# Optimization experiments

Hardware: AMD Instinct MI355X
Metric: run time of the kernel (lower is better)

Reference implementation:

```python
import jax, jax.numpy as jnp
import numpy as np

N = 4096
IN_C = 256
F = 256          # num_filter
C = 40           # label_dim
KP1 = 3          # K+1 Chebyshev orders (K=2 hardcoded in forward)
E = 131072
TWO_PI = 2.0 * np.pi


def build_Lc(edges, q, edge_weight, n):
    """Conjugate of the normalized magnetic Laplacian (max_eigen=2 => L = -A_n * exp(i*Theta)).
    We return conj(L) because the original code swaps L.real/L.imag when feeding `process`,
    which is algebraically O_i = i * conj(T_i(L))."""
    row, col = edges[0], edges[1]
    A = jnp.zeros((n, n), jnp.float32).at[row, col].add(edge_weight)  # duplicates sum, as in coo_matrix
    A_sym = 0.5 * (A + A.T)
    d = A_sym.sum(axis=0)
    d = jnp.where(d == 0, 1.0, d)
    dinv = d ** -0.5
    A_n = dinv[:, None] * A_sym * dinv[None, :]
    Theta = TWO_PI * q * (A - A.T)
    # conj(L) = -A_n * exp(-i*Theta)
    return (-A_n).astype(jnp.complex64) * jnp.exp(-1j * Theta.astype(jnp.complex64))


def cheb_layer(Lc, Xr, Xi, W, b):
    """One ChebConv_Qin_Direct layer. Output = sum_i (i * T_i(conj(L)) @ Xc) @ W_i + bias,
    which reproduces the real/imag-swapped `process` of the original module."""
    Xc = (Xr + 1j * Xi).astype(jnp.complex64)      # [N, d]
    Z0 = Xc
    Z1 = Lc @ Xc                                   # sparse-equivalent spmm, dense here
    Z2 = 2.0 * (Lc @ Z1) - Z0                      # Chebyshev recursion T2 = 2 L T1 - T0
    Yc = 1j * (Z0 @ W[0].astype(jnp.complex64)
               + Z1 @ W[1].astype(jnp.complex64)
               + Z2 @ W[2].astype(jnp.complex64))  # [N, out]
    return Yc.real + b, Yc.imag + b


def setup_inputs() -> dict:
    key = jax.random.key(0)
    k = jax.random.split(key, 8)
    stdv1 = 1.0 / np.sqrt(F)
    return {
        "real": jax.random.normal(k[0], (N, IN_C), jnp.float32),
        "imag": jax.random.normal(k[1], (N, IN_C), jnp.float32),
        "edges": jax.random.randint(k[2], (2, E), 0, N),
        "q": jnp.float32(0.25),
        "edge_weight": jax.random.uniform(k[3], (E,), jnp.float32),
        "W1": jax.random.uniform(k[4], (KP1, IN_C, F), jnp.float32, -stdv1, stdv1),
        "b1": jnp.zeros((1, F), jnp.float32),
        "W2": jax.random.uniform(k[5], (KP1, F, F), jnp.float32, -stdv1, stdv1),
        "b2": jnp.zeros((1, F), jnp.float32),
        "Wc": jax.random.normal(k[6], (C, 2 * F), jnp.float32) * (1.0 / np.sqrt(2 * F)),
        "bc": jnp.zeros((C,), jnp.float32),
    }


def reference(real, imag, edges, q, edge_weight, W1, b1, W2, b2, Wc, bc):
    n = real.shape[0]
    Lc = build_Lc(edges, q, edge_weight, n)        # same L is rebuilt each layer in the original
    r, i = cheb_layer(Lc, real, imag, W1, b1)
    r, i = cheb_layer(Lc, r, i, W2, b2)            # activation=False, dropout=False
    x = jnp.concatenate([r, i], axis=-1)           # [N, 2F]
    logits = x @ Wc.T + bc                         # Conv1d(kernel_size=1) == linear
    return jax.nn.log_softmax(logits, axis=-1)     # [N, C]
```

## Files before the change

kernel.cpp:

```cpp
#include <hip/hip_runtime.h>
#include <cmath>

#define N_NODES 4096
#define FDIM    256
#define CDIM    40
#define NEDGE   131072
#define CAP     256
#define HBITS   19
#define HSIZE   (1 << HBITS)
#define TWO_PI_F 6.28318530717958647692f

typedef __bf16 bf16;
typedef __bf16 bf16x2 __attribute__((ext_vector_type(2)));
typedef __bf16 bf16x4 __attribute__((ext_vector_type(4)));
typedef __bf16 bf16x8 __attribute__((ext_vector_type(8)));
typedef _Float16 f16;
typedef _Float16 f16x2 __attribute__((ext_vector_type(2)));
typedef float  f32x4  __attribute__((ext_vector_type(4)));
typedef unsigned char u8;

static constexpr size_t NF = (size_t)N_NODES * FDIM;

struct __align__(16) Entry { unsigned ab, ba; int col, pad; };

__device__ __forceinline__ unsigned pack_h2(float a, float b) {
    f16x2 h; h[0] = (f16)a; h[1] = (f16)b;
    return __builtin_bit_cast(unsigned, h);
}
__device__ __forceinline__ f16x2 bch2(unsigned u) {
    return __builtin_bit_cast(f16x2, u);
}

__device__ __forceinline__ unsigned f32_to_e5m2(float v) {
    unsigned short h = __builtin_bit_cast(unsigned short, (f16)v);
    return ((unsigned)h + 0x7Fu + (((unsigned)h >> 8) & 1u)) >> 8 & 0xFFu;
}

__device__ __forceinline__ f16x2 e5m2_pair_lo(unsigned u) {
    return bch2(__builtin_amdgcn_perm(u, 0u, 0x05000400u));
}
__device__ __forceinline__ f16x2 e5m2_pair_hi(unsigned u) {
    return bch2(__builtin_amdgcn_perm(u, 0u, 0x07000600u));
}

__device__ __forceinline__ float fdot2(f16x2 a, f16x2 b, float c) {
#if __has_builtin(__builtin_amdgcn_fdot2)
    return __builtin_amdgcn_fdot2(a, b, c, false);
#else
    asm("v_dot2_f32_f16 %0, %1, %2, %0" : "+v"(c) : "v"(a), "v"(b));
    return c;
#endif
}

__device__ __forceinline__ void gld_lds16(const bf16* g, bf16* s) {
    __builtin_amdgcn_global_load_lds(
        (const __attribute__((address_space(1))) void*)g,
        (__attribute__((address_space(3))) void*)s,
        16, 0, 0);
}

__device__ __forceinline__ unsigned cell_hash(unsigned cell) {
    return (cell * 2654435761u) >> (32 - HBITS);
}

__global__ void hash_insert(const int* __restrict__ edges,
                            const float* __restrict__ ew,
                            int* __restrict__ hkey, float* __restrict__ hval,
                            float* __restrict__ rowsum, float* __restrict__ colsum) {
    int e = blockIdx.x * blockDim.x + threadIdx.x;
    if (e >= NEDGE) return;
    int r = edges[e], c = edges[NEDGE + e];
    float wv = ew[e];
    atomicAdd(rowsum + r, wv);
    atomicAdd(colsum + c, wv);
    unsigned cell = (unsigned)r * N_NODES + c;
    unsigned h = cell_hash(cell);
    for (;;) {
        int old = atomicCAS(hkey + h, 0, (int)(cell + 1));
        if (old == 0 || old == (int)(cell + 1)) { atomicAdd(hval + h, wv); break; }
        h = (h + 1) & (HSIZE - 1);
    }
}

__global__ __launch_bounds__(256) void hash_to_ell(
    const int* __restrict__ hkey, const float* __restrict__ hval,
    const float* __restrict__ rowsum, const float* __restrict__ colsum,
    const float* __restrict__ qptr,
    int* __restrict__ cnt, Entry* __restrict__ ent) {
    int h = blockIdx.x * 256 + threadIdx.x;
    int k = hkey[h];
    if (k == 0) return;
    unsigned cell = (unsigned)(k - 1);
    int i = cell >> 12, j = cell & 4095;
    float a = hval[h];
    float b = 0.f;
    bool mirror = false;
    if (i == j) { b = a; mirror = true; }
    else {
        unsigned mcell = (unsigned)j * N_NODES + i;
        unsigned hh = cell_hash(mcell);
        for (;;) {
            int kk = hkey[hh];
            if (kk == (int)(mcell + 1)) { b = hval[hh]; mirror = true; break; }
            if (kk == 0) break;
            hh = (hh + 1) & (HSIZE - 1);
        }
    }
    float di = 0.5f * (rowsum[i] + colsum[i]); if (di == 0.f) di = 1.f;
    float dj = 0.5f * (rowsum[j] + colsum[j]); if (dj == 0.f) dj = 1.f;
    float an = 0.5f * (a + b) / sqrtf(di * dj);
    float s, c;
    sincosf(TWO_PI_F * qptr[0] * (a - b), &s, &c);
    float lr = -an * c;
    float li = an * s;
    int pos = atomicAdd(cnt + i, 1);
    if (pos < CAP) {
        Entry en; en.ab = pack_h2(lr, -li); en.ba = pack_h2(li, lr);
        en.col = j; en.pad = 0;
        ent[(size_t)i * CAP + pos] = en;
    }
    if (!mirror) {
        int pos2 = atomicAdd(cnt + j, 1);
        if (pos2 < CAP) {
            Entry en; en.ab = pack_h2(lr, li); en.ba = pack_h2(-li, lr);
            en.col = i; en.pad = 0;
            ent[(size_t)j * CAP + pos2] = en;
        }
    }
}

#define NWT (256 * 768)
#define CAST_W_BLOCKS ((2 * NWT + 48 * 512) / 256)
__global__ __launch_bounds__(256) void cast_all(
    const float* __restrict__ Xr, const float* __restrict__ Xi,
    const float* __restrict__ W1, const float* __restrict__ W2,
    const float* __restrict__ Wc,
    bf16* __restrict__ Xr16, bf16* __restrict__ Xi16, u8* __restrict__ XC8,
    bf16* __restrict__ W1t, bf16* __restrict__ W2t, bf16* __restrict__ Wcb) {
    int bid = blockIdx.x;
    if (bid < (int)(NF / 256)) {
        int idx = bid * 256 + threadIdx.x;
        float vr = Xr[idx], vi = Xi[idx];
        Xr16[idx] = (bf16)vr; Xi16[idx] = (bf16)vi;
        unsigned pr = f32_to_e5m2(vr), pi = f32_to_e5m2(vi);
        ((unsigned short*)XC8)[idx] = (unsigned short)(pr | (pi << 8));
    } else {
        int idx = (bid - (int)(NF / 256)) * 256 + threadIdx.x;
        if (idx < 2 * NWT) {
            const float* W = (idx < NWT) ? W1 : W2;
            bf16* Wt = (idx < NWT) ? W1t : W2t;
            int id = (idx < NWT) ? idx : idx - NWT;
            int nout = id / 768, kk = id - nout * 768;
            int o = kk >> 8, k = kk & 255;
            Wt[id] = (bf16)W[((size_t)o * 256 + k) * 256 + nout];
        } else {
            int id = idx - 2 * NWT;
            int row = id >> 9, k = id & 511;
            Wcb[id] = (row < CDIM) ? (bf16)Wc[row * 512 + k] : (bf16)0.f;
        }
    }
}

__global__ __launch_bounds__(256) void spmm_k(
    const int* __restrict__ cnt, const Entry* __restrict__ ent,
    const u8* __restrict__ XC8,
    const bf16* __restrict__ C0r, const bf16* __restrict__ C0i,
    float alpha, float beta,
    bf16* __restrict__ Zr, bf16* __restrict__ Zi, u8* __restrict__ ZC8)
{
    __shared__ f32x4 redR[3][64];
    __shared__ f32x4 redI[3][64];

    const int wave = threadIdx.x >> 6, lane = threadIdx.x & 63;
    const int row = blockIdx.x;
    int n1 = cnt[row]; if (n1 > CAP) n1 = CAP;
    const Entry* erow = ent + (size_t)row * CAP;

    float ar[4] = {}, ai[4] = {};
    int e = wave;
    for (; e + 12 < n1; e += 16) {
        Entry e0 = erow[e];
        Entry e1 = erow[e + 4];
        Entry e2 = erow[e + 8];
        Entry e3 = erow[e + 12];
        uint2 x0 = *(const uint2*)&XC8[(size_t)(e0.col & 4095) * 512 + lane * 8];
        uint2 x1 = *(const uint2*)&XC8[(size_t)(e1.col & 4095) * 512 + lane * 8];
        uint2 x2 = *(const uint2*)&XC8[(size_t)(e2.col & 4095) * 512 + lane * 8];
        uint2 x3 = *(const uint2*)&XC8[(size_t)(e3.col & 4095) * 512 + lane * 8];
        {
            f16x2 ab = bch2(e0.ab), ba = bch2(e0.ba);
            f16x2 c0 = e5m2_pair_lo(x0.x), c1 = e5m2_pair_hi(x0.x);
            f16x2 c2 = e5m2_pair_lo(x0.y), c3 = e5m2_pair_hi(x0.y);
            ar[0] = fdot2(ab, c0, ar[0]); ai[0] = fdot2(ba, c0, ai[0]);
            ar[1] = fdot2(ab, c1, ar[1]); ai[1] = fdot2(ba, c1, ai[1]);
            ar[2] = fdot2(ab, c2, ar[2]); ai[2] = fdot2(ba, c2, ai[2]);
            ar[3] = fdot2(ab, c3, ar[3]); ai[3] = fdot2(ba, c3, ai[3]);
        }
        {
            f16x2 ab = bch2(e1.ab), ba = bch2(e1.ba);
            f16x2 c0 = e5m2_pair_lo(x1.x), c1 = e5m2_pair_hi(x1.x);
            f16x2 c2 = e5m2_pair_lo(x1.y), c3 = e5m2_pair_hi(x1.y);
            ar[0] = fdot2(ab, c0, ar[0]); ai[0] = fdot2(ba, c0, ai[0]);
            ar[1] = fdot2(ab, c1, ar[1]); ai[1] = fdot2(ba, c1, ai[1]);
            ar[2] = fdot2(ab, c2, ar[2]); ai[2] = fdot2(ba, c2, ai[2]);
            ar[3] = fdot2(ab, c3, ar[3]); ai[3] = fdot2(ba, c3, ai[3]);
        }
        {
            f16x2 ab = bch2(e2.ab), ba = bch2(e2.ba);
            f16x2 c0 = e5m2_pair_lo(x2.x), c1 = e5m2_pair_hi(x2.x);
            f16x2 c2 = e5m2_pair_lo(x2.y), c3 = e5m2_pair_hi(x2.y);
            ar[0] = fdot2(ab, c0, ar[0]); ai[0] = fdot2(ba, c0, ai[0]);
            ar[1] = fdot2(ab, c1, ar[1]); ai[1] = fdot2(ba, c1, ai[1]);
            ar[2] = fdot2(ab, c2, ar[2]); ai[2] = fdot2(ba, c2, ai[2]);
            ar[3] = fdot2(ab, c3, ar[3]); ai[3] = fdot2(ba, c3, ai[3]);
        }
        {
            f16x2 ab = bch2(e3.ab), ba = bch2(e3.ba);
            f16x2 c0 = e5m2_pair_lo(x3.x), c1 = e5m2_pair_hi(x3.x);
            f16x2 c2 = e5m2_pair_lo(x3.y), c3 = e5m2_pair_hi(x3.y);
            ar[0] = fdot2(ab, c0, ar[0]); ai[0] = fdot2(ba, c0, ai[0]);
            ar[1] = fdot2(ab, c1, ar[1]); ai[1] = fdot2(ba, c1, ai[1]);
            ar[2] = fdot2(ab, c2, ar[2]); ai[2] = fdot2(ba, c2, ai[2]);
            ar[3] = fdot2(ab, c3, ar[3]); ai[3] = fdot2(ba, c3, ai[3]);
        }
    }
    for (; e < n1; e += 4) {
        Entry e0 = erow[e];
        uint2 x0 = *(const uint2*)&XC8[(size_t)(e0.col & 4095) * 512 + lane * 8];
        f16x2 ab = bch2(e0.ab), ba = bch2(e0.ba);
        f16x2 c0 = e5m2_pair_lo(x0.x), c1 = e5m2_pair_hi(x0.x);
        f16x2 c2 = e5m2_pair_lo(x0.y), c3 = e5m2_pair_hi(x0.y);
        ar[0] = fdot2(ab, c0, ar[0]); ai[0] = fdot2(ba, c0, ai[0]);
        ar[1] = fdot2(ab, c1, ar[1]); ai[1] = fdot2(ba, c1, ai[1]);
        ar[2] = fdot2(ab, c2, ar[2]); ai[2] = fdot2(ba, c2, ai[2]);
        ar[3] = fdot2(ab, c3, ar[3]); ai[3] = fdot2(ba, c3, ai[3]);
    }

    if (wave != 0) {
        f32x4 r, i;
        #pragma unroll
        for (int c = 0; c < 4; ++c) { r[c] = ar[c]; i[c] = ai[c]; }
        redR[wave - 1][lane] = r;
        redI[wave - 1][lane] = i;
    }
    __syncthreads();
    if (wave != 0) return;

    #pragma unroll
    for (int w = 0; w < 3; ++w) {
        f32x4 r = redR[w][lane], i = redI[w][lane];
        #pragma unroll
        for (int c = 0; c < 4; ++c) { ar[c] += r[c]; ai[c] += i[c]; }
    }

    size_t pbase = (size_t)row * FDIM + lane * 4;
    float vr[4], vi[4];
    if (beta != 0.f) {
        bf16x4 cr = *(const bf16x4*)&C0r[pbase];
        bf16x4 ci = *(const bf16x4*)&C0i[pbase];
        #pragma unroll
        for (int c = 0; c < 4; ++c) {
            vr[c] = alpha * ar[c] + beta * (float)cr[c];
            vi[c] = alpha * ai[c] + beta * (float)ci[c];
        }
    } else {
        #pragma unroll
        for (int c = 0; c < 4; ++c) { vr[c] = alpha * ar[c]; vi[c] = alpha * ai[c]; }
    }
    bf16x4 pr, pi;
    #pragma unroll
    for (int c = 0; c < 4; ++c) { pr[c] = (bf16)vr[c]; pi[c] = (bf16)vi[c]; }
    *(bf16x4*)&Zr[pbase] = pr;
    *(bf16x4*)&Zi[pbase] = pi;
    if (ZC8) {
        uint2 o;
        o.x = f32_to_e5m2(vr[0]) | (f32_to_e5m2(vi[0]) << 8) |
              (f32_to_e5m2(vr[1]) << 16) | (f32_to_e5m2(vi[1]) << 24);
        o.y = f32_to_e5m2(vr[2]) | (f32_to_e5m2(vi[2]) << 8) |
              (f32_to_e5m2(vr[3]) << 16) | (f32_to_e5m2(vi[3]) << 24);
        *(uint2*)&ZC8[(size_t)row * 512 + lane * 8] = o;
    }
}

__global__ __launch_bounds__(256) void wapply_mfma(
    const bf16* __restrict__ Z0r, const bf16* __restrict__ Z0i,
    const bf16* __restrict__ Z1r, const bf16* __restrict__ Z1i,
    const bf16* __restrict__ Z2r, const bf16* __restrict__ Z2i,
    const bf16* __restrict__ Wt,
    const float* __restrict__ bias,
    bf16* __restrict__ O16r_r, bf16* __restrict__ O16r_i,
    u8* __restrict__ OC8)
{
    __shared__ __align__(16) bf16 sZr[32 * 32];
    __shared__ __align__(16) bf16 sZi[32 * 32];
    __shared__ __align__(16) bf16 sW [64 * 32];

    const int tid  = threadIdx.x;
    const int wave = tid >> 6;
    const int lane = tid & 63;
    const int rowBase = blockIdx.y * 32;
    const int colBase = blockIdx.x * 64;

    const int srow = lane >> 2;
    const int skc  = (lane & 3) * 8;

    f32x4 accSr[2] = {}, accSi[2] = {};
    const int fr = lane & 15;
    const int fk = (lane >> 4) * 8;

    for (int kb = 0; kb < 3 * FDIM; kb += 32) {
        int order = kb >> 8;
        int kloc  = kb & 255;
        if (wave == 0 || wave == 1) {
            const bf16* z;
            if (wave == 0) z = (order == 0) ? Z0r : (order == 1) ? Z1r : Z2r;
            else           z = (order == 0) ? Z0i : (order == 1) ? Z1i : Z2i;
            bf16* s = (wave == 0) ? sZr : sZi;
            const bf16* g = z + (size_t)(rowBase + srow) * FDIM + kloc + skc;
            #pragma unroll
            for (int t = 0; t < 2; ++t)
                gld_lds16(g + (size_t)t * 16 * FDIM, s + t * 512);
        } else if (wave == 2) {
            const bf16* g = Wt + (size_t)(colBase + srow) * 768 + kb + skc;
            #pragma unroll
            for (int t = 0; t < 4; ++t)
                gld_lds16(g + (size_t)t * 16 * 768, sW + t * 512);
        }
        __syncthreads();

        bf16x8 zr[2], zi[2], wv;
        #pragma unroll
        for (int m = 0; m < 2; ++m) {
            int r = m * 16 + fr;
            zr[m] = *(const bf16x8*)&sZr[r * 32 + fk];
            zi[m] = *(const bf16x8*)&sZi[r * 32 + fk];
        }
        wv = *(const bf16x8*)&sW[(wave * 16 + fr) * 32 + fk];
        #pragma unroll
        for (int m = 0; m < 2; ++m) {
            accSr[m] = __builtin_amdgcn_mfma_f32_16x16x32_bf16(zr[m], wv, accSr[m], 0, 0, 0);
            accSi[m] = __builtin_amdgcn_mfma_f32_16x16x32_bf16(zi[m], wv, accSi[m], 0, 0, 0);
        }
        __syncthreads();
    }

    #pragma unroll
    for (int m = 0; m < 2; ++m) {
        int row0 = rowBase + m * 16 + (lane >> 4) * 4;
        int col  = colBase + wave * 16 + fr;
        float bv = bias[col];
        #pragma unroll
        for (int r = 0; r < 4; ++r) {
            float vr = bv - accSi[m][r];
            float vi = bv + accSr[m][r];
            int row = row0 + r;
            size_t idx = (size_t)row * FDIM + col;
            if (O16r_r) {
                O16r_r[idx] = (bf16)vr; O16r_i[idx] = (bf16)vi;
            }
            if (OC8) {
                unsigned pr = f32_to_e5m2(vr), pi = f32_to_e5m2(vi);
                ((unsigned short*)OC8)[idx] = (unsigned short)(pr | (pi << 8));
            }
        }
    }
}

__global__ __launch_bounds__(256) void head_mfma(
    const bf16* __restrict__ Yrb,
    const bf16* __restrict__ Yib,
    const bf16* __restrict__ Wcb,
    const float* __restrict__ bc,
    float* __restrict__ out)
{
    __shared__ __align__(16) bf16 sY[64][72];
    __shared__ __align__(16) bf16 sW[48][72];
    __shared__ float sS[64][52];

    const int tid  = threadIdx.x;
    const int wave = tid >> 6;
    const int lane = tid & 63;
    const int r0 = blockIdx.x * 64;

    f32x4 acc[3] = {};

    for (int kb = 0; kb < 512; kb += 64) {
        const bf16* src = (kb < 256) ? Yrb : Yib;
        const int koff = kb & 255;
        #pragma unroll
        for (int e = 0; e < 2; ++e) {
            int idx = tid + e * 256;
            int rr = idx >> 3, kk = (idx & 7) * 8;
            *(bf16x8*)&sY[rr][kk] =
                *(const bf16x8*)&src[(size_t)(r0 + rr) * FDIM + koff + kk];
        }
        #pragma unroll
        for (int e = 0; e < 2; ++e) {
            int idx = tid + e * 256;
            if (idx < 384) {
                int rr = idx >> 3, kk = (idx & 7) * 8;
                *(bf16x8*)&sW[rr][kk] =
                    *(const bf16x8*)&Wcb[(size_t)rr * 512 + kb + kk];
            }
        }
        __syncthreads();
        #pragma unroll
        for (int ks = 0; ks < 2; ++ks) {
            bf16x8 a = *(const bf16x8*)&sY[wave * 16 + (lane & 15)][ks * 32 + (lane >> 4) * 8];
            #pragma unroll
            for (int n = 0; n < 3; ++n) {
                bf16x8 b = *(const bf16x8*)&sW[n * 16 + (lane & 15)][ks * 32 + (lane >> 4) * 8];
                acc[n] = __builtin_amdgcn_mfma_f32_16x16x32_bf16(a, b, acc[n], 0, 0, 0);
            }
        }
        __syncthreads();
    }

    #pragma unroll
    for (int n = 0; n < 3; ++n) {
        int col = n * 16 + (lane & 15);
        int rloc = wave * 16 + (lane >> 4) * 4;
        #pragma unroll
        for (int r = 0; r < 4; ++r)
            sS[rloc + r][col] = acc[n][r];
    }
    __syncthreads();

    if (tid < 64) {
        float mx = -INFINITY;
        #pragma unroll 8
        for (int c = 0; c < CDIM; ++c) {
            float lv = sS[tid][c] + bc[c];
            sS[tid][c] = lv;
            mx = fmaxf(mx, lv);
        }
        float se = 0.f;
        #pragma unroll 8
        for (int c = 0; c < CDIM; ++c) se += expf(sS[tid][c] - mx);
        float lse = mx + logf(se);
        #pragma unroll 8
        for (int c = 0; c < CDIM; ++c)
            out[(size_t)(r0 + tid) * CDIM + c] = sS[tid][c] - lse;
    }
}

extern "C" void kernel_launch(void* const* d_in, const int* in_sizes, int n_in,
                              void* d_out, int out_size, void* d_ws, size_t ws_size,
                              hipStream_t stream) {
    const float* real = (const float*)d_in[0];
    const float* imag = (const float*)d_in[1];
    const int*   edges = (const int*)d_in[2];
    const float* q    = (const float*)d_in[3];
    const float* ew   = (const float*)d_in[4];
    const float* W1   = (const float*)d_in[5];
    const float* b1   = (const float*)d_in[6];
    const float* W2   = (const float*)d_in[7];
    const float* b2   = (const float*)d_in[8];
    const float* Wc   = (const float*)d_in[9];
    const float* bc   = (const float*)d_in[10];
    float* out = (float*)d_out;

    char* w = (char*)d_ws;
    int*      hkey   = (int*)w;   w += (size_t)HSIZE * 4;
    float*    hval   = (float*)w; w += (size_t)HSIZE * 4;
    int*      cnt    = (int*)w;   w += N_NODES * 4;
    float*    rowsum = (float*)w; w += N_NODES * 4;
    float*    colsum = (float*)w; w += N_NODES * 4;
    size_t zero_bytes = (size_t)((char*)w - (char*)d_ws);
    Entry* ent  = (Entry*)w; w += (size_t)N_NODES * CAP * 16;
    bf16* Xr16 = (bf16*)w; w += NF * 2;
    bf16* Xi16 = (bf16*)w; w += NF * 2;
    u8*   XC8  = (u8*)w;   w += NF * 2;
    bf16* Z1r  = (bf16*)w; w += NF * 2;
    bf16* Z1i  = (bf16*)w; w += NF * 2;
    u8*   Z1C8 = (u8*)w;   w += NF * 2;
    bf16* Z2r  = (bf16*)w; w += NF * 2;
    bf16* Z2i  = (bf16*)w; w += NF * 2;
    bf16* Y1rb = (bf16*)w; w += NF * 2;
    bf16* Y1ib = (bf16*)w; w += NF * 2;
    u8*   Y1C8 = (u8*)w;   w += NF * 2;
    bf16* Y2rb = (bf16*)w; w += NF * 2;
    bf16* Y2ib = (bf16*)w; w += NF * 2;
    bf16* W1t  = (bf16*)w; w += 256 * 768 * 2;
    bf16* W2t  = (bf16*)w; w += 256 * 768 * 2;
    bf16* Wcb  = (bf16*)w; w += 48 * 512 * 2;

    hipMemsetAsync(d_ws, 0, zero_bytes, stream);

    hash_insert<<<(NEDGE + 255) / 256, 256, 0, stream>>>(edges, ew, hkey, hval,
                                                         rowsum, colsum);
    hash_to_ell<<<HSIZE / 256, 256, 0, stream>>>(hkey, hval, rowsum, colsum,
                                                 q, cnt, ent);

    cast_all<<<(int)(NF / 256) + CAST_W_BLOCKS, 256, 0, stream>>>(
        real, imag, W1, W2, Wc, Xr16, Xi16, XC8, W1t, W2t, Wcb);

    dim3 gW(FDIM / 64, N_NODES / 32);

    spmm_k<<<N_NODES, 256, 0, stream>>>(cnt, ent, XC8, nullptr, nullptr,
                                        1.f, 0.f, Z1r, Z1i, Z1C8);
    spmm_k<<<N_NODES, 256, 0, stream>>>(cnt, ent, Z1C8, Xr16, Xi16,
                                        2.f, -1.f, Z2r, Z2i, nullptr);
    wapply_mfma<<<gW, 256, 0, stream>>>(Xr16, Xi16, Z1r, Z1i, Z2r, Z2i,
                                        W1t, b1,
                                        Y1rb, Y1ib,
                                        Y1C8);

    spmm_k<<<N_NODES, 256, 0, stream>>>(cnt, ent, Y1C8, nullptr, nullptr,
                                        1.f, 0.f, Z1r, Z1i, Z1C8);
    spmm_k<<<N_NODES, 256, 0, stream>>>(cnt, ent, Z1C8, Y1rb, Y1ib,
                                        2.f, -1.f, Z2r, Z2i, nullptr);
    wapply_mfma<<<gW, 256, 0, stream>>>(Y1rb, Y1ib, Z1r, Z1i, Z2r, Z2i,
                                        W2t, b2,
                                        Y2rb, Y2ib,
                                        nullptr);

    head_mfma<<<64, 256, 0, stream>>>(Y2rb, Y2ib, Wcb, bc, out);
}
```

Measured before the change: 265.3 us.

## Merge hash insert with casts and stage ELL rows in LDS for spmm

Merges the hash-insert kernel and the input/weight cast kernel into one launch so both run concurrently and one launch is saved. In spmm, each block copies its row's ELL entries into shared memory with direct global-to-LDS loads, then reads entries from LDS. The inner loop is unrolled to 8 entries per wave so more neighbor gathers are in flight. This adds a barrier and more registers per thread, which may lower occupancy. The LDS copy has a row-capacity assumption: every wave whose base index is below the row count loads a full 64 entries, so partially filled tails bring in unused slots.

```diff
diff --git a/kernel.cpp b/kernel.cpp
--- a/kernel.cpp
+++ b/kernel.cpp
@@ -52,7 +52,7 @@
 #endif
 }
 
-__device__ __forceinline__ void gld_lds16(const bf16* g, bf16* s) {
+__device__ __forceinline__ void gld_lds16(const void* g, void* s) {
     __builtin_amdgcn_global_load_lds(
         (const __attribute__((address_space(1))) void*)g,
         (__attribute__((address_space(3))) void*)s,
@@ -63,22 +63,54 @@
     return (cell * 2654435761u) >> (32 - HBITS);
 }
 
-__global__ void hash_insert(const int* __restrict__ edges,
-                            const float* __restrict__ ew,
-                            int* __restrict__ hkey, float* __restrict__ hval,
-                            float* __restrict__ rowsum, float* __restrict__ colsum) {
-    int e = blockIdx.x * blockDim.x + threadIdx.x;
-    if (e >= NEDGE) return;
-    int r = edges[e], c = edges[NEDGE + e];
-    float wv = ew[e];
-    atomicAdd(rowsum + r, wv);
-    atomicAdd(colsum + c, wv);
-    unsigned cell = (unsigned)r * N_NODES + c;
-    unsigned h = cell_hash(cell);
-    for (;;) {
-        int old = atomicCAS(hkey + h, 0, (int)(cell + 1));
-        if (old == 0 || old == (int)(cell + 1)) { atomicAdd(hval + h, wv); break; }
-        h = (h + 1) & (HSIZE - 1);
+#define NWT (256 * 768)
+#define HASH_BLOCKS ((NEDGE + 255) / 256)
+#define XCAST_BLOCKS ((int)(NF / 256))
+#define WCAST_BLOCKS ((2 * NWT + 48 * 512) / 256)
+__global__ __launch_bounds__(256) void prep_k(
+    const int* __restrict__ edges, const float* __restrict__ ew,
+    int* __restrict__ hkey, float* __restrict__ hval,
+    float* __restrict__ rowsum, float* __restrict__ colsum,
+    const float* __restrict__ Xr, const float* __restrict__ Xi,
+    const float* __restrict__ W1, const float* __restrict__ W2,
+    const float* __restrict__ Wc,
+    bf16* __restrict__ Xr16, bf16* __restrict__ Xi16, u8* __restrict__ XC8,
+    bf16* __restrict__ W1t, bf16* __restrict__ W2t, bf16* __restrict__ Wcb) {
+    int bid = blockIdx.x;
+    if (bid < HASH_BLOCKS) {
+        int e = bid * 256 + threadIdx.x;
+        if (e >= NEDGE) return;
+        int r = edges[e], c = edges[NEDGE + e];
+        float wv = ew[e];
+        atomicAdd(rowsum + r, wv);
+        atomicAdd(colsum + c, wv);
+        unsigned cell = (unsigned)r * N_NODES + c;
+        unsigned h = cell_hash(cell);
+        for (;;) {
+            int old = atomicCAS(hkey + h, 0, (int)(cell + 1));
+            if (old == 0 || old == (int)(cell + 1)) { atomicAdd(hval + h, wv); break; }
+            h = (h + 1) & (HSIZE - 1);
+        }
+    } else if (bid < HASH_BLOCKS + XCAST_BLOCKS) {
+        int idx = (bid - HASH_BLOCKS) * 256 + threadIdx.x;
+        float vr = Xr[idx], vi = Xi[idx];
+        Xr16[idx] = (bf16)vr; Xi16[idx] = (bf16)vi;
+        unsigned pr = f32_to_e5m2(vr), pi = f32_to_e5m2(vi);
+        ((unsigned short*)XC8)[idx] = (unsigned short)(pr | (pi << 8));
+    } else {
+        int idx = (bid - HASH_BLOCKS - XCAST_BLOCKS) * 256 + threadIdx.x;
+        if (idx < 2 * NWT) {
+            const float* W = (idx < NWT) ? W1 : W2;
+            bf16* Wt = (idx < NWT) ? W1t : W2t;
+            int id = (idx < NWT) ? idx : idx - NWT;
+            int nout = id / 768, kk = id - nout * 768;
+            int o = kk >> 8, k = kk & 255;
+            Wt[id] = (bf16)W[((size_t)o * 256 + k) * 256 + nout];
+        } else {
+            int id = idx - 2 * NWT;
+            int row = id >> 9, k = id & 511;
+            Wcb[id] = (row < CDIM) ? (bf16)Wc[row * 512 + k] : (bf16)0.f;
+        }
     }
 }
 
@@ -129,38 +161,6 @@
     }
 }
 
-#define NWT (256 * 768)
-#define CAST_W_BLOCKS ((2 * NWT + 48 * 512) / 256)
-__global__ __launch_bounds__(256) void cast_all(
-    const float* __restrict__ Xr, const float* __restrict__ Xi,
-    const float* __restrict__ W1, const float* __restrict__ W2,
-    const float* __restrict__ Wc,
-    bf16* __restrict__ Xr16, bf16* __restrict__ Xi16, u8* __restrict__ XC8,
-    bf16* __restrict__ W1t, bf16* __restrict__ W2t, bf16* __restrict__ Wcb) {
-    int bid = blockIdx.x;
-    if (bid < (int)(NF / 256)) {
-        int idx = bid * 256 + threadIdx.x;
-        float vr = Xr[idx], vi = Xi[idx];
-        Xr16[idx] = (bf16)vr; Xi16[idx] = (bf16)vi;
-        unsigned pr = f32_to_e5m2(vr), pi = f32_to_e5m2(vi);
-        ((unsigned short*)XC8)[idx] = (unsigned short)(pr | (pi << 8));
-    } else {
-        int idx = (bid - (int)(NF / 256)) * 256 + threadIdx.x;
-        if (idx < 2 * NWT) {
-            const float* W = (idx < NWT) ? W1 : W2;
-            bf16* Wt = (idx < NWT) ? W1t : W2t;
-            int id = (idx < NWT) ? idx : idx - NWT;
-            int nout = id / 768, kk = id - nout * 768;
-            int o = kk >> 8, k = kk & 255;
-            Wt[id] = (bf16)W[((size_t)o * 256 + k) * 256 + nout];
-        } else {
-            int id = idx - 2 * NWT;
-            int row = id >> 9, k = id & 511;
-            Wcb[id] = (row < CDIM) ? (bf16)Wc[row * 512 + k] : (bf16)0.f;
-        }
-    }
-}
-
 __global__ __launch_bounds__(256) void spmm_k(
     const int* __restrict__ cnt, const Entry* __restrict__ ent,
     const u8* __restrict__ XC8,
@@ -168,6 +168,7 @@
     float alpha, float beta,
     bf16* __restrict__ Zr, bf16* __restrict__ Zi, u8* __restrict__ ZC8)
 {
+    __shared__ __align__(16) Entry sent[CAP];
     __shared__ f32x4 redR[3][64];
     __shared__ f32x4 redI[3][64];
 
@@ -176,56 +177,34 @@
     int n1 = cnt[row]; if (n1 > CAP) n1 = CAP;
     const Entry* erow = ent + (size_t)row * CAP;
 
+    if (wave * 64 < n1)
+        gld_lds16(erow + wave * 64 + lane, sent + wave * 64);
+    __syncthreads();
+
     float ar[4] = {}, ai[4] = {};
     int e = wave;
-    for (; e + 12 < n1; e += 16) {
-        Entry e0 = erow[e];
-        Entry e1 = erow[e + 4];
-        Entry e2 = erow[e + 8];
-        Entry e3 = erow[e + 12];
-        uint2 x0 = *(const uint2*)&XC8[(size_t)(e0.col & 4095) * 512 + lane * 8];
-        uint2 x1 = *(const uint2*)&XC8[(size_t)(e1.col & 4095) * 512 + lane * 8];
-        uint2 x2 = *(const uint2*)&XC8[(size_t)(e2.col & 4095) * 512 + lane * 8];
-        uint2 x3 = *(const uint2*)&XC8[(size_t)(e3.col & 4095) * 512 + lane * 8];
-        {
-            f16x2 ab = bch2(e0.ab), ba = bch2(e0.ba);
-            f16x2 c0 = e5m2_pair_lo(x0.x), c1 = e5m2_pair_hi(x0.x);
-            f16x2 c2 = e5m2_pair_lo(x0.y), c3 = e5m2_pair_hi(x0.y);
+    for (; e + 28 < n1; e += 32) {
+        Entry ee[8];
+        #pragma unroll
+        for (int u = 0; u < 8; ++u)
+            ee[u] = sent[e + 4 * u];
+        uint2 xv[8];
+        #pragma unroll
+        for (int u = 0; u < 8; ++u)
+            xv[u] = *(const uint2*)&XC8[(size_t)(ee[u].col & 4095) * 512 + lane * 8];
+        #pragma unroll
+        for (int u = 0; u < 8; ++u) {
+            f16x2 ab = bch2(ee[u].ab), ba = bch2(ee[u].ba);
+            f16x2 c0 = e5m2_pair_lo(xv[u].x), c1 = e5m2_pair_hi(xv[u].x);
+            f16x2 c2 = e5m2_pair_lo(xv[u].y), c3 = e5m2_pair_hi(xv[u].y);
             ar[0] = fdot2(ab, c0, ar[0]); ai[0] = fdot2(ba, c0, ai[0]);
             ar[1] = fdot2(ab, c1, ar[1]); ai[1] = fdot2(ba, c1, ai[1]);
             ar[2] = fdot2(ab, c2, ar[2]); ai[2] = fdot2(ba, c2, ai[2]);
             ar[3] = fdot2(ab, c3, ar[3]); ai[3] = fdot2(ba, c3, ai[3]);
         }
-        {
-            f16x2 ab = bch2(e1.ab), ba = bch2(e1.ba);
-            f16x2 c0 = e5m2_pair_lo(x1.x), c1 = e5m2_pair_hi(x1.x);
-            f16x2 c2 = e5m2_pair_lo(x1.y), c3 = e5m2_pair_hi(x1.y);
-            ar[0] = fdot2(ab, c0, ar[0]); ai[0] = fdot2(ba, c0, ai[0]);
-            ar[1] = fdot2(ab, c1, ar[1]); ai[1] = fdot2(ba, c1, ai[1]);
-            ar[2] = fdot2(ab, c2, ar[2]); ai[2] = fdot2(ba, c2, ai[2]);
-            ar[3] = fdot2(ab, c3, ar[3]); ai[3] = fdot2(ba, c3, ai[3]);
-        }
-        {
-            f16x2 ab = bch2(e2.ab), ba = bch2(e2.ba);
-            f16x2 c0 = e5m2_pair_lo(x2.x), c1 = e5m2_pair_hi(x2.x);
-            f16x2 c2 = e5m2_pair_lo(x2.y), c3 = e5m2_pair_hi(x2.y);
-            ar[0] = fdot2(ab, c0, ar[0]); ai[0] = fdot2(ba, c0, ai[0]);
-            ar[1] = fdot2(ab, c1, ar[1]); ai[1] = fdot2(ba, c1, ai[1]);
-            ar[2] = fdot2(ab, c2, ar[2]); ai[2] = fdot2(ba, c2, ai[2]);
-            ar[3] = fdot2(ab, c3, ar[3]); ai[3] = fdot2(ba, c3, ai[3]);
-        }
-        {
-            f16x2 ab = bch2(e3.ab), ba = bch2(e3.ba);
-            f16x2 c0 = e5m2_pair_lo(x3.x), c1 = e5m2_pair_hi(x3.x);
-            f16x2 c2 = e5m2_pair_lo(x3.y), c3 = e5m2_pair_hi(x3.y);
-            ar[0] = fdot2(ab, c0, ar[0]); ai[0] = fdot2(ba, c0, ai[0]);
-            ar[1] = fdot2(ab, c1, ar[1]); ai[1] = fdot2(ba, c1, ai[1]);
-            ar[2] = fdot2(ab, c2, ar[2]); ai[2] = fdot2(ba, c2, ai[2]);
-            ar[3] = fdot2(ab, c3, ar[3]); ai[3] = fdot2(ba, c3, ai[3]);
-        }
     }
     for (; e < n1; e += 4) {
-        Entry e0 = erow[e];
+        Entry e0 = sent[e];
         uint2 x0 = *(const uint2*)&XC8[(size_t)(e0.col & 4095) * 512 + lane * 8];
         f16x2 ab = bch2(e0.ab), ba = bch2(e0.ba);
         f16x2 c0 = e5m2_pair_lo(x0.x), c1 = e5m2_pair_hi(x0.x);
@@ -487,13 +466,13 @@
 
     hipMemsetAsync(d_ws, 0, zero_bytes, stream);
 
-    hash_insert<<<(NEDGE + 255) / 256, 256, 0, stream>>>(edges, ew, hkey, hval,
-                                                         rowsum, colsum);
+    prep_k<<<HASH_BLOCKS + XCAST_BLOCKS + WCAST_BLOCKS, 256, 0, stream>>>(
+        edges, ew, hkey, hval, rowsum, colsum,
+        real, imag, W1, W2, Wc,
+        Xr16, Xi16, XC8, W1t, W2t, Wcb);
+
     hash_to_ell<<<HSIZE / 256, 256, 0, stream>>>(hkey, hval, rowsum, colsum,
                                                  q, cnt, ent);
-
-    cast_all<<<(int)(NF / 256) + CAST_W_BLOCKS, 256, 0, stream>>>(
-        real, imag, W1, W2, Wc, Xr16, Xi16, XC8, W1t, W2t, Wcb);
 
     dim3 gW(FDIM / 64, N_NODES / 32);
 
```

Measured after the change: 236.6 us. 10.8% less time.
